# Performance work log

Measured on AMD Instinct MI355X. Metric: run time of the kernel, lower is better.

## Reference

```python
import jax, jax.numpy as jnp
import numpy as np
from jax.scipy.linalg import expm

D_LOGIC = 128
D_MEM = 16
SO_DIM = D_MEM * (D_MEM - 1) // 2  # 120


def _linear_init(key, fan_in, shape):
    bound = 1.0 / np.sqrt(fan_in)
    return jax.random.uniform(key, shape, jnp.float32, -bound, bound)


def setup_inputs() -> dict:
    key = jax.random.key(0)
    ks = jax.random.split(key, 14)
    B, S = 4, 128
    return {
        "x_logic": jax.random.normal(ks[0], (B, S, D_LOGIC), jnp.float32),
        "x_memory": jax.random.normal(ks[1], (B, S, D_MEM), jnp.float32),
        # W_Q / W_K
        "Wq": _linear_init(ks[2], D_LOGIC, (D_LOGIC, D_LOGIC)),
        "bq": _linear_init(ks[3], D_LOGIC, (D_LOGIC,)),
        "Wk": _linear_init(ks[4], D_LOGIC, (D_LOGIC, D_LOGIC)),
        "bk": _linear_init(ks[5], D_LOGIC, (D_LOGIC,)),
        # gamma_net: Linear(d_logic, 2*d_logic) -> Tanh -> Linear(2*d_logic, so_dim)
        "W1": _linear_init(ks[6], D_LOGIC, (2 * D_LOGIC, D_LOGIC)),
        "b1": _linear_init(ks[7], D_LOGIC, (2 * D_LOGIC,)),
        "W2": _linear_init(ks[8], 2 * D_LOGIC, (SO_DIM, 2 * D_LOGIC)),
        "b2": _linear_init(ks[9], 2 * D_LOGIC, (SO_DIM,)),
        # out_proj: Linear(d_memory, d_memory)
        "Wo": _linear_init(ks[10], D_MEM, (D_MEM, D_MEM)),
        "bo": _linear_init(ks[11], D_MEM, (D_MEM,)),
    }


def reference(x_logic, x_memory, Wq, bq, Wk, bk, W1, b1, W2, b2, Wo, bo):
    B, S, d_logic = x_logic.shape
    dm = x_memory.shape[-1]

    # attention over logic stream
    Q = x_logic @ Wq.T + bq
    K = x_logic @ Wk.T + bk
    attn = jax.nn.softmax(
        jnp.einsum("bjd,bid->bji", Q, K) / jnp.sqrt(jnp.float32(d_logic)), axis=-1
    )  # [B, S(j), S(i)]

    # per-pair Lie-algebra params: delta[b,j,i] = x_logic[b,j] - x_logic[b,i]
    delta = x_logic[:, :, None, :] - x_logic[:, None, :, :]  # [B,S,S,d_logic]
    h = jnp.tanh(delta @ W1.T + b1)
    lie = h @ W2.T + b2  # [B,S,S,so_dim]

    # scatter into skew-symmetric matrices [B,S,S,dm,dm]
    r, c = np.triu_indices(dm, k=1)
    skew = jnp.zeros((B, S, S, dm, dm), x_logic.dtype)
    skew = skew.at[..., r, c].set(lie)
    skew = skew.at[..., c, r].set(-lie)

    # Lie-group exponential -> orthogonal transport matrices
    T_all = expm(skew)  # [B,S,S,dm,dm]

    # transported[b,j,i,:] = T[b,j,i] @ x_memory[b,i]
    transported = jnp.einsum("bjide,bie->bjid", T_all, x_memory)

    # attention-weighted aggregation over i
    settled = jnp.einsum("bji,bjid->bjd", attn, transported)  # [B,S,dm]

    out = settled @ Wo.T + bo
    return out, T_all
```

## Files before the change

kernel.cpp:

```cpp
#include <hip/hip_runtime.h>
#include <hip/hip_fp16.h>

#define S_LEN 128
#define DLOG  128
#define DMEM  16
#define SO    120
#define HDIM  256

typedef _Float16 v8h __attribute__((ext_vector_type(8)));
typedef __fp16 v2hf __attribute__((ext_vector_type(2)));
typedef float v4f __attribute__((ext_vector_type(4)));

union PkU { v2hf h; unsigned u; };
union V8U { v8h v; int u[4]; };

__device__ __forceinline__ v8h splat8(float x) {
  _Float16 h = (_Float16)x;
  v8h v = {h, h, h, h, h, h, h, h};
  return v;
}

__global__ __launch_bounds__(512) void qku_kernel(
    const float* __restrict__ xl, const float* __restrict__ Wq,
    const float* __restrict__ bq, const float* __restrict__ Wk,
    const float* __restrict__ bk, const float* __restrict__ W1,
    float* __restrict__ Q, float* __restrict__ K, float* __restrict__ u) {
  int bj = blockIdx.x, t = threadIdx.x;
  int lane = t & 63, wu = t >> 6;
  int half = lane >> 5, l5 = lane & 31;
  float4 xv = *(const float4*)(xl + bj * 128 + 4 * l5);
  int seg = wu >> 1;
  const float* wb;
  if (seg == 0) wb = Wq;
  else if (seg == 1) wb = Wk - 128 * 128;
  else wb = W1 - 256 * 128;
  #pragma unroll 4
  for (int step = 0; step < 32; ++step) {
    int ro = wu * 64 + 2 * step + half;
    float4 wv = *(const float4*)(wb + ro * 128 + 4 * l5);
    float v = fmaf(wv.x, xv.x, fmaf(wv.y, xv.y, fmaf(wv.z, xv.z, wv.w * xv.w)));
    v += __shfl_xor(v, 1, 64);
    v += __shfl_xor(v, 2, 64);
    v += __shfl_xor(v, 4, 64);
    v += __shfl_xor(v, 8, 64);
    v += __shfl_xor(v, 16, 64);
    if (l5 == 0) {
      if (seg == 0) Q[bj * 128 + ro] = v + bq[ro];
      else if (seg == 1) K[bj * 128 + (ro - 128)] = v + bk[ro - 128];
      else u[bj * 256 + (ro - 256)] = v;
    }
  }
}

__global__ __launch_bounds__(128) void attn_kernel(
    const float* __restrict__ Q, const float* __restrict__ K,
    float* __restrict__ attn) {
  int bj = blockIdx.x, b = bj >> 7, t = threadIdx.x;
  int lane = t & 63, wu = t >> 6;
  int half = lane >> 5, l5 = lane & 31;
  __shared__ float sc[128];
  __shared__ float red[128];
  float4 qv = *(const float4*)(Q + bj * 128 + 4 * l5);
  #pragma unroll 4
  for (int step = 0; step < 32; ++step) {
    int ro = wu * 64 + 2 * step + half;
    float4 kv = *(const float4*)(K + (size_t)(b * 128 + ro) * 128 + 4 * l5);
    float v = fmaf(kv.x, qv.x, fmaf(kv.y, qv.y, fmaf(kv.z, qv.z, kv.w * qv.w)));
    v += __shfl_xor(v, 1, 64);
    v += __shfl_xor(v, 2, 64);
    v += __shfl_xor(v, 4, 64);
    v += __shfl_xor(v, 8, 64);
    v += __shfl_xor(v, 16, 64);
    if (l5 == 0) sc[ro] = v * 0.08838834764831845f;
  }
  __syncthreads();
  int i = t;
  float s = sc[i];
  red[i] = s;
  __syncthreads();
  for (int off = 64; off; off >>= 1) {
    if (i < off) red[i] = fmaxf(red[i], red[i + off]);
    __syncthreads();
  }
  float m = red[0];
  __syncthreads();
  float e = expf(s - m);
  red[i] = e;
  __syncthreads();
  for (int off = 64; off; off >>= 1) {
    if (i < off) red[i] += red[i + off];
    __syncthreads();
  }
  attn[(size_t)bj * 128 + i] = e / red[0];
}

__global__ __launch_bounds__(256) void h_from_u_kernel(
    const float* __restrict__ u, const float* __restrict__ b1,
    _Float16* __restrict__ hG, const float* __restrict__ W2g,
    _Float16* __restrict__ w2h) {
  if (blockIdx.x >= 2048) {
    int idx = ((blockIdx.x - 2048) * 256 + threadIdx.x) * 4;
    float4 v = *(const float4*)(W2g + idx);
    PkU u0, u1;
    u0.h = __builtin_amdgcn_cvt_pkrtz(v.x, v.y);
    u1.h = __builtin_amdgcn_cvt_pkrtz(v.z, v.w);
    uint2 pk = {u0.u, u1.u};
    *(uint2*)(w2h + idx) = pk;
    return;
  }
  int tid = blockIdx.x * 256 + threadIdx.x;
  #pragma unroll
  for (int g = 0; g < 4; ++g) {
    int unit = tid + g * 524288;
    int p = unit >> 5;
    int o0 = (unit & 31) * 8;
    int bj = p >> 7;
    int b = bj >> 7;
    int i = p & 127;
    const float* uj = u + bj * 256 + o0;
    const float* ui = u + (size_t)(b * 128 + i) * 256 + o0;
    const float* bb = b1 + o0;
    float4 j0 = *(const float4*)uj, j1 = *(const float4*)(uj + 4);
    float4 i0 = *(const float4*)ui, i1 = *(const float4*)(ui + 4);
    float4 c0 = *(const float4*)bb, c1 = *(const float4*)(bb + 4);
    float xv[8] = {j0.x - i0.x + c0.x, j0.y - i0.y + c0.y,
                   j0.z - i0.z + c0.z, j0.w - i0.w + c0.w,
                   j1.x - i1.x + c1.x, j1.y - i1.y + c1.y,
                   j1.z - i1.z + c1.z, j1.w - i1.w + c1.w};
    float rv[8];
    #pragma unroll
    for (int k = 0; k < 8; ++k) {
      float x = xv[k];
      float ax = fabsf(x);
      float e = __expf(-2.f * ax);
      float r = __fdividef(1.f - e, 1.f + e);
      rv[k] = copysignf(r, x);
    }
    V8U out;
    #pragma unroll
    for (int k = 0; k < 4; ++k) {
      PkU pu;
      pu.h = __builtin_amdgcn_cvt_pkrtz(rv[2 * k], rv[2 * k + 1]);
      out.u[k] = (int)pu.u;
    }
    *(v8h*)(hG + (size_t)p * 512 + o0) = out.v;
  }
}

__global__ __launch_bounds__(512) void lie_kernel(
    const _Float16* __restrict__ w2h, const float* __restrict__ b2g,
    float* __restrict__ Tg) {
  __shared__ _Float16 w2t[128 * 136];
  int t = threadIdx.x, lane = t & 63;
  int wu = __builtin_amdgcn_readfirstlane(t >> 6);
  int pbase = blockIdx.x * 128 + wu * 16;
  int nn = lane & 15, q = lane >> 4;
  const _Float16* hf = (const _Float16*)Tg;

  for (int idx = t; idx < 1088; idx += 512) w2t[16320 + idx] = (_Float16)0.f;

  v4f acc[8];
  #pragma unroll
  for (int tt = 0; tt < 8; ++tt) acc[tt] = (v4f){0.f, 0.f, 0.f, 0.f};

  const _Float16* hrow = hf + (size_t)(pbase + nn) * 512;
  for (int khalf = 0; khalf < 2; ++khalf) {
    __syncthreads();
    for (int idx = t; idx < 1920; idx += 512) {
      int row = idx >> 4, cu = (idx & 15) * 8;
      *(v8h*)(w2t + row * 136 + cu) =
          *(const v8h*)(w2h + row * 256 + khalf * 128 + cu);
    }
    __syncthreads();
    #pragma unroll
    for (int ks = 0; ks < 4; ++ks) {
      v8h ah = *(const v8h*)(hrow + khalf * 128 + ks * 32 + 8 * q);
      #pragma unroll
      for (int tt = 0; tt < 8; ++tt) {
        const v8h bf = *(const v8h*)(w2t + (16 * tt + nn) * 136 + ks * 32 + 8 * q);
        acc[tt] = __builtin_amdgcn_mfma_f32_16x16x32_f16(ah, bf, acc[tt], 0, 0, 0);
      }
    }
  }

  int rc0[8], rc1[8];
  float bbv[8];
  bool val[8];
  #pragma unroll
  for (int tt = 0; tt < 8; ++tt) {
    int n16 = 16 * tt + nn;
    val[tt] = (n16 < 120);
    float fr_ = floorf((31.0f - sqrtf(961.0f - 8.0f * (float)n16)) * 0.5f);
    int r = (int)fr_;
    int Sr = 15 * r - ((r * (r - 1)) >> 1);
    int c = n16 - Sr + r + 1;
    rc0[tt] = r * 16 + c;
    rc1[tt] = c * 16 + r;
    bbv[tt] = val[tt] ? b2g[n16] : 0.f;
  }

  _Float16* hw = (_Float16*)Tg;
  _Float16* aSt = w2t;
  for (int pass = 0; pass < 2; ++pass) {
    __syncthreads();
    #pragma unroll
    for (int reg = 0; reg < 4; ++reg) {
      int pidx = 4 * q + reg;
      if ((pidx >> 3) == pass) {
        _Float16* ab = aSt + (wu * 8 + (pidx & 7)) * 256;
        #pragma unroll
        for (int tt = 0; tt < 8; ++tt) {
          if (val[tt]) {
            _Float16 hv = (_Float16)(acc[tt][reg] + bbv[tt]);
            ab[rc0[tt]] = hv;
            ab[rc1[tt]] = -hv;
          }
        }
        ab[nn * 17] = (_Float16)0.f;
      }
    }
    __syncthreads();
    #pragma unroll
    for (int k = 0; k < 4; ++k) {
      int unit = t + k * 512;
      int lp = unit >> 5, off = (unit & 31) * 8;
      int g = blockIdx.x * 128 + (lp >> 3) * 16 + pass * 8 + (lp & 7);
      *(v8h*)(hw + (size_t)g * 512 + 256 + off) = *(const v8h*)(aSt + lp * 256 + off);
    }
  }
}

__device__ __forceinline__ void split8(const float* x, v8h& hi, v8h& lo) {
  union U { v8h v; v2hf p[4]; } H, L;
  #pragma unroll
  for (int i = 0; i < 4; ++i) {
    float a = x[2 * i], b = x[2 * i + 1];
    v2hf h = __builtin_amdgcn_cvt_pkrtz(a, b);
    float ra = (float)h[0], rb = (float)h[1];
    v2hf l = __builtin_amdgcn_cvt_pkrtz(a - ra, b - rb);
    H.p[i] = h;
    L.p[i] = l;
  }
  hi = H.v;
  lo = L.v;
}

__global__ __launch_bounds__(256) void expm_kernel(
    float* __restrict__ Tg, const float* __restrict__ attn,
    const float* __restrict__ xm, float* __restrict__ part) {
  __shared__ char lds[10240] __attribute__((aligned(16)));
  __shared__ float sred[4][16];
  int t = threadIdx.x, lane = t & 63;
  int wu = __builtin_amdgcn_readfirstlane(t >> 6);
  int pbase = blockIdx.x * 8 + wu * 2;
  int nn = lane & 15, q = lane >> 4, b8 = (q & 1) * 8;
  float* ErB = (float*)(lds + wu * 2560);
  const _Float16* hf = (const _Float16*)Tg;

  int idxA = ((2 * (q & 1)) * 16 + nn) * 4;
  int idxB = idxA + 64;

  float scv[2];
  int sv[2];
  V8U Apk[2], BfA[2];
  v4f Af[2];
  #pragma unroll
  for (int j = 0; j < 2; ++j) {
    size_t p = (size_t)(pbase + j);
    const _Float16* Ap = hf + p * 512 + 256;
    v8h rowh = *(const v8h*)(Ap + nn * 16 + b8);
    float s2 = 0.f;
    #pragma unroll
    for (int k = 0; k < 8; ++k) {
      float xf = (float)rowh[k];
      s2 = fmaf(xf, xf, s2);
    }
    #pragma unroll
    for (int off = 1; off < 64; off <<= 1) s2 += __shfl_xor(s2, off, 64);
    float bound = 0.5f * sqrtf(s2);
    int s = 0;
    while (bound > 1.0f && s < 12) { bound *= 0.5f; s++; }
    sv[j] = __builtin_amdgcn_readfirstlane(s);
    scv[j] = ldexpf(1.0f, -s);
    v8h sch = splat8(scv[j]);
    V8U ap;
    ap.v = rowh * sch;
    #pragma unroll
    for (int i = 0; i < 4; ++i) {
      Apk[j].u[i] = ap.u[i];
      BfA[j].u[i] = ap.u[i] ^ 0x80008000;
    }
    #pragma unroll
    for (int reg = 0; reg < 4; ++reg)
      Af[j][reg] = (float)Ap[(4 * q + reg) * 16 + nn] * scv[j];
  }

  V8U IC1, IC2;
  #pragma unroll
  for (int i = 0; i < 4; ++i) {
    float d0 = (b8 + 2 * i == nn) ? 1.f : 0.f;
    float d1 = (b8 + 2 * i + 1 == nn) ? 1.f : 0.f;
    PkU u1, u2;
    u1.h = __builtin_amdgcn_cvt_pkrtz(10.666667f * d0, 10.666667f * d1);
    u2.h = __builtin_amdgcn_cvt_pkrtz(2.1333333f * d0, 2.1333333f * d1);
    IC1.u[i] = (int)u1.u;
    IC2.u[i] = (int)u2.u;
  }

  v4f z4 = {0.f, 0.f, 0.f, 0.f};

  v4f cB[2];
  #pragma unroll
  for (int j = 0; j < 2; ++j)
    cB[j] = __builtin_amdgcn_mfma_f32_16x16x32_f16(Apk[j].v, BfA[j].v, z4, 0, 0, 0);

  V8U fB[2];
  #pragma unroll
  for (int j = 0; j < 2; ++j) {
    PkU u0, u1;
    u0.h = __builtin_amdgcn_cvt_pkrtz(cB[j][0], cB[j][1]);
    u1.h = __builtin_amdgcn_cvt_pkrtz(cB[j][2], cB[j][3]);
    fB[j].u[0] = __builtin_amdgcn_ds_bpermute(idxA, (int)u0.u);
    fB[j].u[1] = __builtin_amdgcn_ds_bpermute(idxA, (int)u1.u);
    fB[j].u[2] = __builtin_amdgcn_ds_bpermute(idxB, (int)u0.u);
    fB[j].u[3] = __builtin_amdgcn_ds_bpermute(idxB, (int)u1.u);
  }

  v4f cB2[2];
  #pragma unroll
  for (int j = 0; j < 2; ++j)
    cB2[j] = __builtin_amdgcn_mfma_f32_16x16x32_f16(fB[j].v, fB[j].v, z4, 0, 0, 0);

  V8U fB2[2];
  #pragma unroll
  for (int j = 0; j < 2; ++j) {
    PkU u0, u1;
    u0.h = __builtin_amdgcn_cvt_pkrtz(cB2[j][0], cB2[j][1]);
    u1.h = __builtin_amdgcn_cvt_pkrtz(cB2[j][2], cB2[j][3]);
    fB2[j].u[0] = __builtin_amdgcn_ds_bpermute(idxA, (int)u0.u);
    fB2[j].u[1] = __builtin_amdgcn_ds_bpermute(idxA, (int)u1.u);
    fB2[j].u[2] = __builtin_amdgcn_ds_bpermute(idxB, (int)u0.u);
    fB2[j].u[3] = __builtin_amdgcn_ds_bpermute(idxB, (int)u1.u);
  }

  v8h k1a = splat8(7.9365079e-4f);
  v8h k1b = splat8(0.17777778f);
  v8h k2a = splat8(8.8183422e-5f);
  v8h k2b = splat8(2.5396825e-2f);
  V8U M1[2], M2[2];
  #pragma unroll
  for (int j = 0; j < 2; ++j) {
    M1[j].v = fB2[j].v * k1a + (fB[j].v * k1b + IC1.v);
    M2[j].v = fB2[j].v * k2a + (fB[j].v * k2b + IC2.v);
  }

  v4f Cc[2], Qc[2];
  #pragma unroll
  for (int j = 0; j < 2; ++j) {
    v4f c3m = __builtin_amdgcn_mfma_f32_16x16x32_f16(M1[j].v, fB2[j].v, z4, 0, 0, 0);
    v4f c4m = __builtin_amdgcn_mfma_f32_16x16x32_f16(M2[j].v, fB2[j].v, z4, 0, 0, 0);
    #pragma unroll
    for (int reg = 0; reg < 4; ++reg) {
      float dg = (4 * q + reg == nn) ? 1.f : 0.f;
      Cc[j][reg] = fmaf(c3m[reg], 2.44140625e-4f,
                        fmaf(cB[j][reg], 0.25f, dg + Af[j][reg]));
      Qc[j][reg] = fmaf(c4m[reg], 2.44140625e-4f, cB[j][reg] * 0.083333333f);
    }
  }

  V8U fQ[2];
  #pragma unroll
  for (int j = 0; j < 2; ++j) {
    PkU u0, u1;
    u0.h = __builtin_amdgcn_cvt_pkrtz(Qc[j][0], Qc[j][1]);
    u1.h = __builtin_amdgcn_cvt_pkrtz(Qc[j][2], Qc[j][3]);
    fQ[j].u[0] = __builtin_amdgcn_ds_bpermute(idxA, (int)u0.u);
    fQ[j].u[1] = __builtin_amdgcn_ds_bpermute(idxA, (int)u1.u);
    fQ[j].u[2] = __builtin_amdgcn_ds_bpermute(idxB, (int)u0.u);
    fQ[j].u[3] = __builtin_amdgcn_ds_bpermute(idxB, (int)u1.u);
  }

  v4f E[2];
  #pragma unroll
  for (int j = 0; j < 2; ++j) {
    v4f c5 = __builtin_amdgcn_mfma_f32_16x16x32_f16(Apk[j].v, fQ[j].v, z4, 0, 0, 0);
    E[j] = Cc[j] + c5 * 0.5f;
  }

  int smax = max(sv[0], sv[1]);
  for (int it = 0; it < smax; ++it) {
    #pragma unroll
    for (int j = 0; j < 2; ++j) {
      if (it < sv[j]) {
        float* Erp = ErB + j * 320;
        PkU u0, u1;
        u0.h = __builtin_amdgcn_cvt_pkrtz(E[j][0], E[j][1]);
        u1.h = __builtin_amdgcn_cvt_pkrtz(E[j][2], E[j][3]);
        V8U bfe;
        bfe.u[0] = __builtin_amdgcn_ds_bpermute(idxA, (int)u0.u);
        bfe.u[1] = __builtin_amdgcn_ds_bpermute(idxA, (int)u1.u);
        bfe.u[2] = __builtin_amdgcn_ds_bpermute(idxB, (int)u0.u);
        bfe.u[3] = __builtin_amdgcn_ds_bpermute(idxB, (int)u1.u);
        #pragma unroll
        for (int reg = 0; reg < 4; ++reg)
          Erp[(4 * q + reg) * 20 + nn] = E[j][reg];
        asm volatile("s_waitcnt lgkmcnt(0)" ::: "memory");
        float4 a0 = *(const float4*)(Erp + nn * 20 + b8);
        float4 a1 = *(const float4*)(Erp + nn * 20 + b8 + 4);
        float xa[8] = {a0.x, a0.y, a0.z, a0.w, a1.x, a1.y, a1.z, a1.w};
        v8h ahi, alo;
        split8(xa, ahi, alo);
        v8h Ecat = (q < 2) ? ahi : alo;
        v4f z = {0.f, 0.f, 0.f, 0.f};
        E[j] = __builtin_amdgcn_mfma_f32_16x16x32_f16(Ecat, bfe.v, z, 0, 0, 0);
      }
    }
  }

  float pacc[4] = {0.f, 0.f, 0.f, 0.f};
  #pragma unroll
  for (int j = 0; j < 2; ++j) {
    int p = pbase + j;
    float* dst = Tg + (size_t)p * 256;
    #pragma unroll
    for (int reg = 0; reg < 4; ++reg)
      dst[(4 * q + reg) * 16 + nn] = E[j][reg];
    int b = p >> 14, i = p & 127;
    float xv = xm[((b << 7) + i) * 16 + nn];
    float aw = attn[(size_t)p] * xv;
    #pragma unroll
    for (int reg = 0; reg < 4; ++reg)
      pacc[reg] = fmaf(aw, E[j][reg], pacc[reg]);
  }
  #pragma unroll
  for (int reg = 0; reg < 4; ++reg) {
    #pragma unroll
    for (int off = 1; off < 16; off <<= 1)
      pacc[reg] += __shfl_xor(pacc[reg], off, 64);
  }
  if (nn == 0) {
    #pragma unroll
    for (int reg = 0; reg < 4; ++reg) sred[wu][4 * q + reg] = pacc[reg];
  }
  __syncthreads();
  if (t < 16)
    part[(size_t)blockIdx.x * 16 + t] =
        sred[0][t] + sred[1][t] + sred[2][t] + sred[3][t];
}

__global__ __launch_bounds__(64) void settle_fin_kernel(
    const float* __restrict__ part, const float* __restrict__ Wo,
    const float* __restrict__ bo, float* __restrict__ outp) {
  int bj = blockIdx.x, t = threadIdx.x;
  int r = t & 15, e0 = t >> 4;
  const float* pb = part + (size_t)bj * 256;
  float s = pb[e0 * 16 + r] + pb[(e0 + 4) * 16 + r] +
            pb[(e0 + 8) * 16 + r] + pb[(e0 + 12) * 16 + r];
  __shared__ float sf[64];
  sf[t] = s;
  __syncthreads();
  if (t < 16) sf[t] = sf[t] + sf[16 + t] + sf[32 + t] + sf[48 + t];
  __syncthreads();
  if (t < 16) {
    float o = bo[t];
    const float* wr = Wo + t * 16;
    #pragma unroll
    for (int c = 0; c < 16; ++c) o = fmaf(wr[c], sf[c], o);
    outp[bj * 16 + t] = o;
  }
}

extern "C" void kernel_launch(void* const* d_in, const int* in_sizes, int n_in,
                              void* d_out, int out_size, void* d_ws,
                              size_t ws_size, hipStream_t stream) {
  const float* xl = (const float*)d_in[0];
  const float* xm = (const float*)d_in[1];
  const float* Wq = (const float*)d_in[2];
  const float* bq = (const float*)d_in[3];
  const float* Wk = (const float*)d_in[4];
  const float* bk = (const float*)d_in[5];
  const float* W1 = (const float*)d_in[6];
  const float* b1 = (const float*)d_in[7];
  const float* W2 = (const float*)d_in[8];
  const float* b2 = (const float*)d_in[9];
  const float* Wo = (const float*)d_in[10];
  const float* bo = (const float*)d_in[11];
  float* outp = (float*)d_out;
  float* Tg = outp + 8192;
  float* wsf = (float*)d_ws;
  float* Q = wsf;
  float* K = wsf + 65536;
  float* attn = wsf + 131072;
  _Float16* w2h = (_Float16*)Q;
  float* u = wsf + 196608;
  float* part = wsf + 196608;

  hipLaunchKernelGGL(qku_kernel, dim3(512), dim3(512), 0, stream, xl, Wq, bq, Wk, bk, W1, Q, K, u);
  hipLaunchKernelGGL(attn_kernel, dim3(512), dim3(128), 0, stream, Q, K, attn);
  hipLaunchKernelGGL(h_from_u_kernel, dim3(2078), dim3(256), 0, stream, u, b1, (_Float16*)Tg, W2, w2h);
  hipLaunchKernelGGL(lie_kernel, dim3(512), dim3(512), 0, stream, w2h, b2, Tg);
  hipLaunchKernelGGL(expm_kernel, dim3(8192), dim3(256), 0, stream, Tg, attn, xm, part);
  hipLaunchKernelGGL(settle_fin_kernel, dim3(512), dim3(64), 0, stream, part, Wo, bo, outp);
}
```

Baseline: 201.6 us.

## Fuse lie projection into expm kernel and merge attention with tanh kernel

Merges the attention softmax and the tanh hidden-activation kernel into one launch, and fuses the W2 projection (lie_kernel) into the matrix-exponential kernel so skew matrices stay in LDS instead of round-tripping through global memory. Each expm block now handles 64 pairs in a loop, converting W2 to fp16 on the fly per block. The scaling bound now also uses an infinity-norm estimate (min with the Frobenius-based bound), which can reduce squaring steps. The cost is redundant W2 loading and conversion per block, plus larger LDS use that may lower occupancy.

```diff
diff --git a/kernel.cpp b/kernel.cpp
--- a/kernel.cpp
+++ b/kernel.cpp
@@ -52,63 +52,53 @@
   }
 }
 
-__global__ __launch_bounds__(128) void attn_kernel(
+__global__ __launch_bounds__(256) void attn_h_kernel(
     const float* __restrict__ Q, const float* __restrict__ K,
-    float* __restrict__ attn) {
-  int bj = blockIdx.x, b = bj >> 7, t = threadIdx.x;
-  int lane = t & 63, wu = t >> 6;
-  int half = lane >> 5, l5 = lane & 31;
-  __shared__ float sc[128];
-  __shared__ float red[128];
-  float4 qv = *(const float4*)(Q + bj * 128 + 4 * l5);
-  #pragma unroll 4
-  for (int step = 0; step < 32; ++step) {
-    int ro = wu * 64 + 2 * step + half;
-    float4 kv = *(const float4*)(K + (size_t)(b * 128 + ro) * 128 + 4 * l5);
-    float v = fmaf(kv.x, qv.x, fmaf(kv.y, qv.y, fmaf(kv.z, qv.z, kv.w * qv.w)));
-    v += __shfl_xor(v, 1, 64);
-    v += __shfl_xor(v, 2, 64);
-    v += __shfl_xor(v, 4, 64);
-    v += __shfl_xor(v, 8, 64);
-    v += __shfl_xor(v, 16, 64);
-    if (l5 == 0) sc[ro] = v * 0.08838834764831845f;
-  }
-  __syncthreads();
-  int i = t;
-  float s = sc[i];
-  red[i] = s;
-  __syncthreads();
-  for (int off = 64; off; off >>= 1) {
-    if (i < off) red[i] = fmaxf(red[i], red[i + off]);
-    __syncthreads();
-  }
-  float m = red[0];
-  __syncthreads();
-  float e = expf(s - m);
-  red[i] = e;
-  __syncthreads();
-  for (int off = 64; off; off >>= 1) {
-    if (i < off) red[i] += red[i + off];
-    __syncthreads();
-  }
-  attn[(size_t)bj * 128 + i] = e / red[0];
-}
-
-__global__ __launch_bounds__(256) void h_from_u_kernel(
-    const float* __restrict__ u, const float* __restrict__ b1,
-    _Float16* __restrict__ hG, const float* __restrict__ W2g,
-    _Float16* __restrict__ w2h) {
-  if (blockIdx.x >= 2048) {
-    int idx = ((blockIdx.x - 2048) * 256 + threadIdx.x) * 4;
-    float4 v = *(const float4*)(W2g + idx);
-    PkU u0, u1;
-    u0.h = __builtin_amdgcn_cvt_pkrtz(v.x, v.y);
-    u1.h = __builtin_amdgcn_cvt_pkrtz(v.z, v.w);
-    uint2 pk = {u0.u, u1.u};
-    *(uint2*)(w2h + idx) = pk;
+    float* __restrict__ attn, const float* __restrict__ u,
+    const float* __restrict__ b1, _Float16* __restrict__ hG) {
+  int t = threadIdx.x;
+  if (blockIdx.x < 256) {
+    int sub = t >> 7, t128 = t & 127;
+    int bj = blockIdx.x * 2 + sub, b = bj >> 7;
+    int lane = t & 63, wu = (t >> 6) & 1;
+    int half = lane >> 5, l5 = lane & 31;
+    __shared__ float sc[2][128];
+    __shared__ float red[2][128];
+    float4 qv = *(const float4*)(Q + bj * 128 + 4 * l5);
+    #pragma unroll 4
+    for (int step = 0; step < 32; ++step) {
+      int ro = wu * 64 + 2 * step + half;
+      float4 kv = *(const float4*)(K + (size_t)(b * 128 + ro) * 128 + 4 * l5);
+      float v = fmaf(kv.x, qv.x, fmaf(kv.y, qv.y, fmaf(kv.z, qv.z, kv.w * qv.w)));
+      v += __shfl_xor(v, 1, 64);
+      v += __shfl_xor(v, 2, 64);
+      v += __shfl_xor(v, 4, 64);
+      v += __shfl_xor(v, 8, 64);
+      v += __shfl_xor(v, 16, 64);
+      if (l5 == 0) sc[sub][ro] = v * 0.08838834764831845f;
+    }
+    __syncthreads();
+    int i = t128;
+    float s = sc[sub][i];
+    red[sub][i] = s;
+    __syncthreads();
+    for (int off = 64; off; off >>= 1) {
+      if (i < off) red[sub][i] = fmaxf(red[sub][i], red[sub][i + off]);
+      __syncthreads();
+    }
+    float m = red[sub][0];
+    __syncthreads();
+    float e = expf(s - m);
+    red[sub][i] = e;
+    __syncthreads();
+    for (int off = 64; off; off >>= 1) {
+      if (i < off) red[sub][i] += red[sub][i + off];
+      __syncthreads();
+    }
+    attn[(size_t)bj * 128 + i] = e / red[sub][0];
     return;
   }
-  int tid = blockIdx.x * 256 + threadIdx.x;
+  int tid = (blockIdx.x - 256) * 256 + t;
   #pragma unroll
   for (int g = 0; g < 4; ++g) {
     int unit = tid + g * 524288;
@@ -147,89 +137,6 @@
   }
 }
 
-__global__ __launch_bounds__(512) void lie_kernel(
-    const _Float16* __restrict__ w2h, const float* __restrict__ b2g,
-    float* __restrict__ Tg) {
-  __shared__ _Float16 w2t[128 * 136];
-  int t = threadIdx.x, lane = t & 63;
-  int wu = __builtin_amdgcn_readfirstlane(t >> 6);
-  int pbase = blockIdx.x * 128 + wu * 16;
-  int nn = lane & 15, q = lane >> 4;
-  const _Float16* hf = (const _Float16*)Tg;
-
-  for (int idx = t; idx < 1088; idx += 512) w2t[16320 + idx] = (_Float16)0.f;
-
-  v4f acc[8];
-  #pragma unroll
-  for (int tt = 0; tt < 8; ++tt) acc[tt] = (v4f){0.f, 0.f, 0.f, 0.f};
-
-  const _Float16* hrow = hf + (size_t)(pbase + nn) * 512;
-  for (int khalf = 0; khalf < 2; ++khalf) {
-    __syncthreads();
-    for (int idx = t; idx < 1920; idx += 512) {
-      int row = idx >> 4, cu = (idx & 15) * 8;
-      *(v8h*)(w2t + row * 136 + cu) =
-          *(const v8h*)(w2h + row * 256 + khalf * 128 + cu);
-    }
-    __syncthreads();
-    #pragma unroll
-    for (int ks = 0; ks < 4; ++ks) {
-      v8h ah = *(const v8h*)(hrow + khalf * 128 + ks * 32 + 8 * q);
-      #pragma unroll
-      for (int tt = 0; tt < 8; ++tt) {
-        const v8h bf = *(const v8h*)(w2t + (16 * tt + nn) * 136 + ks * 32 + 8 * q);
-        acc[tt] = __builtin_amdgcn_mfma_f32_16x16x32_f16(ah, bf, acc[tt], 0, 0, 0);
-      }
-    }
-  }
-
-  int rc0[8], rc1[8];
-  float bbv[8];
-  bool val[8];
-  #pragma unroll
-  for (int tt = 0; tt < 8; ++tt) {
-    int n16 = 16 * tt + nn;
-    val[tt] = (n16 < 120);
-    float fr_ = floorf((31.0f - sqrtf(961.0f - 8.0f * (float)n16)) * 0.5f);
-    int r = (int)fr_;
-    int Sr = 15 * r - ((r * (r - 1)) >> 1);
-    int c = n16 - Sr + r + 1;
-    rc0[tt] = r * 16 + c;
-    rc1[tt] = c * 16 + r;
-    bbv[tt] = val[tt] ? b2g[n16] : 0.f;
-  }
-
-  _Float16* hw = (_Float16*)Tg;
-  _Float16* aSt = w2t;
-  for (int pass = 0; pass < 2; ++pass) {
-    __syncthreads();
-    #pragma unroll
-    for (int reg = 0; reg < 4; ++reg) {
-      int pidx = 4 * q + reg;
-      if ((pidx >> 3) == pass) {
-        _Float16* ab = aSt + (wu * 8 + (pidx & 7)) * 256;
-        #pragma unroll
-        for (int tt = 0; tt < 8; ++tt) {
-          if (val[tt]) {
-            _Float16 hv = (_Float16)(acc[tt][reg] + bbv[tt]);
-            ab[rc0[tt]] = hv;
-            ab[rc1[tt]] = -hv;
-          }
-        }
-        ab[nn * 17] = (_Float16)0.f;
-      }
-    }
-    __syncthreads();
-    #pragma unroll
-    for (int k = 0; k < 4; ++k) {
-      int unit = t + k * 512;
-      int lp = unit >> 5, off = (unit & 31) * 8;
-      int g = blockIdx.x * 128 + (lp >> 3) * 16 + pass * 8 + (lp & 7);
-      *(v8h*)(hw + (size_t)g * 512 + 256 + off) = *(const v8h*)(aSt + lp * 256 + off);
-    }
-  }
-}
-
 __device__ __forceinline__ void split8(const float* x, v8h& hi, v8h& lo) {
   union U { v8h v; v2hf p[4]; } H, L;
   #pragma unroll
@@ -245,55 +152,76 @@
   lo = L.v;
 }
 
-__global__ __launch_bounds__(256) void expm_kernel(
+__global__ __launch_bounds__(256) void lie_expm_kernel(
+    const float* __restrict__ W2g, const float* __restrict__ b2g,
     float* __restrict__ Tg, const float* __restrict__ attn,
     const float* __restrict__ xm, float* __restrict__ part) {
-  __shared__ char lds[10240] __attribute__((aligned(16)));
+  __shared__ _Float16 w2t[128 * 136];
+  __shared__ float ErB_all[4 * 640];
   __shared__ float sred[4][16];
   int t = threadIdx.x, lane = t & 63;
   int wu = __builtin_amdgcn_readfirstlane(t >> 6);
-  int pbase = blockIdx.x * 8 + wu * 2;
   int nn = lane & 15, q = lane >> 4, b8 = (q & 1) * 8;
-  float* ErB = (float*)(lds + wu * 2560);
+  int gbase = blockIdx.x * 64;
   const _Float16* hf = (const _Float16*)Tg;
+
+  for (int idx = t; idx < 1088; idx += 256) w2t[16320 + idx] = (_Float16)0.f;
+
+  v4f acc[8];
+  #pragma unroll
+  for (int tt = 0; tt < 8; ++tt) acc[tt] = (v4f){0.f, 0.f, 0.f, 0.f};
+
+  const _Float16* hrow = hf + (size_t)(gbase + wu * 16 + nn) * 512;
+  for (int khalf = 0; khalf < 2; ++khalf) {
+    __syncthreads();
+    for (int idx = t; idx < 3840; idx += 256) {
+      int row = idx >> 5, c4 = (idx & 31) * 4;
+      float4 v = *(const float4*)(W2g + row * 256 + khalf * 128 + c4);
+      PkU a, b;
+      a.h = __builtin_amdgcn_cvt_pkrtz(v.x, v.y);
+      b.h = __builtin_amdgcn_cvt_pkrtz(v.z, v.w);
+      uint2 pk = {a.u, b.u};
+      *(uint2*)(w2t + row * 136 + c4) = pk;
+    }
+    __syncthreads();
+    #pragma unroll
+    for (int ks = 0; ks < 4; ++ks) {
+      v8h ah = *(const v8h*)(hrow + khalf * 128 + ks * 32 + 8 * q);
+      #pragma unroll
+      for (int tt = 0; tt < 8; ++tt) {
+        const v8h bf = *(const v8h*)(w2t + (16 * tt + nn) * 136 + ks * 32 + 8 * q);
+        acc[tt] = __builtin_amdgcn_mfma_f32_16x16x32_f16(ah, bf, acc[tt], 0, 0, 0);
+      }
+    }
+  }
+
+  __syncthreads();
+  _Float16* A = w2t;
+  #pragma unroll
+  for (int tt = 0; tt < 8; ++tt) {
+    int n16 = 16 * tt + nn;
+    if (n16 < 120) {
+      float bb = b2g[n16];
+      float fr_ = floorf((31.0f - sqrtf(961.0f - 8.0f * (float)n16)) * 0.5f);
+      int r = (int)fr_;
+      int Sr = 15 * r - ((r * (r - 1)) >> 1);
+      int c = n16 - Sr + r + 1;
+      #pragma unroll
+      for (int reg = 0; reg < 4; ++reg) {
+        int lp = wu * 16 + 4 * q + reg;
+        _Float16 hv = (_Float16)(acc[tt][reg] + bb);
+        A[lp * 256 + r * 16 + c] = hv;
+        A[lp * 256 + c * 16 + r] = -hv;
+      }
+    }
+  }
+  #pragma unroll
+  for (int reg = 0; reg < 4; ++reg)
+    A[(wu * 16 + 4 * q + reg) * 256 + nn * 17] = (_Float16)0.f;
 
   int idxA = ((2 * (q & 1)) * 16 + nn) * 4;
   int idxB = idxA + 64;
-
-  float scv[2];
-  int sv[2];
-  V8U Apk[2], BfA[2];
-  v4f Af[2];
-  #pragma unroll
-  for (int j = 0; j < 2; ++j) {
-    size_t p = (size_t)(pbase + j);
-    const _Float16* Ap = hf + p * 512 + 256;
-    v8h rowh = *(const v8h*)(Ap + nn * 16 + b8);
-    float s2 = 0.f;
-    #pragma unroll
-    for (int k = 0; k < 8; ++k) {
-      float xf = (float)rowh[k];
-      s2 = fmaf(xf, xf, s2);
-    }
-    #pragma unroll
-    for (int off = 1; off < 64; off <<= 1) s2 += __shfl_xor(s2, off, 64);
-    float bound = 0.5f * sqrtf(s2);
-    int s = 0;
-    while (bound > 1.0f && s < 12) { bound *= 0.5f; s++; }
-    sv[j] = __builtin_amdgcn_readfirstlane(s);
-    scv[j] = ldexpf(1.0f, -s);
-    v8h sch = splat8(scv[j]);
-    V8U ap;
-    ap.v = rowh * sch;
-    #pragma unroll
-    for (int i = 0; i < 4; ++i) {
-      Apk[j].u[i] = ap.u[i];
-      BfA[j].u[i] = ap.u[i] ^ 0x80008000;
-    }
-    #pragma unroll
-    for (int reg = 0; reg < 4; ++reg)
-      Af[j][reg] = (float)Ap[(4 * q + reg) * 16 + nn] * scv[j];
-  }
+  float* ErW = ErB_all + wu * 640;
 
   V8U IC1, IC2;
   #pragma unroll
@@ -306,132 +234,177 @@
     IC1.u[i] = (int)u1.u;
     IC2.u[i] = (int)u2.u;
   }
-
-  v4f z4 = {0.f, 0.f, 0.f, 0.f};
-
-  v4f cB[2];
-  #pragma unroll
-  for (int j = 0; j < 2; ++j)
-    cB[j] = __builtin_amdgcn_mfma_f32_16x16x32_f16(Apk[j].v, BfA[j].v, z4, 0, 0, 0);
-
-  V8U fB[2];
-  #pragma unroll
-  for (int j = 0; j < 2; ++j) {
-    PkU u0, u1;
-    u0.h = __builtin_amdgcn_cvt_pkrtz(cB[j][0], cB[j][1]);
-    u1.h = __builtin_amdgcn_cvt_pkrtz(cB[j][2], cB[j][3]);
-    fB[j].u[0] = __builtin_amdgcn_ds_bpermute(idxA, (int)u0.u);
-    fB[j].u[1] = __builtin_amdgcn_ds_bpermute(idxA, (int)u1.u);
-    fB[j].u[2] = __builtin_amdgcn_ds_bpermute(idxB, (int)u0.u);
-    fB[j].u[3] = __builtin_amdgcn_ds_bpermute(idxB, (int)u1.u);
-  }
-
-  v4f cB2[2];
-  #pragma unroll
-  for (int j = 0; j < 2; ++j)
-    cB2[j] = __builtin_amdgcn_mfma_f32_16x16x32_f16(fB[j].v, fB[j].v, z4, 0, 0, 0);
-
-  V8U fB2[2];
-  #pragma unroll
-  for (int j = 0; j < 2; ++j) {
-    PkU u0, u1;
-    u0.h = __builtin_amdgcn_cvt_pkrtz(cB2[j][0], cB2[j][1]);
-    u1.h = __builtin_amdgcn_cvt_pkrtz(cB2[j][2], cB2[j][3]);
-    fB2[j].u[0] = __builtin_amdgcn_ds_bpermute(idxA, (int)u0.u);
-    fB2[j].u[1] = __builtin_amdgcn_ds_bpermute(idxA, (int)u1.u);
-    fB2[j].u[2] = __builtin_amdgcn_ds_bpermute(idxB, (int)u0.u);
-    fB2[j].u[3] = __builtin_amdgcn_ds_bpermute(idxB, (int)u1.u);
-  }
-
   v8h k1a = splat8(7.9365079e-4f);
   v8h k1b = splat8(0.17777778f);
   v8h k2a = splat8(8.8183422e-5f);
   v8h k2b = splat8(2.5396825e-2f);
-  V8U M1[2], M2[2];
-  #pragma unroll
-  for (int j = 0; j < 2; ++j) {
-    M1[j].v = fB2[j].v * k1a + (fB[j].v * k1b + IC1.v);
-    M2[j].v = fB2[j].v * k2a + (fB[j].v * k2b + IC2.v);
-  }
-
-  v4f Cc[2], Qc[2];
-  #pragma unroll
-  for (int j = 0; j < 2; ++j) {
-    v4f c3m = __builtin_amdgcn_mfma_f32_16x16x32_f16(M1[j].v, fB2[j].v, z4, 0, 0, 0);
-    v4f c4m = __builtin_amdgcn_mfma_f32_16x16x32_f16(M2[j].v, fB2[j].v, z4, 0, 0, 0);
-    #pragma unroll
-    for (int reg = 0; reg < 4; ++reg) {
-      float dg = (4 * q + reg == nn) ? 1.f : 0.f;
-      Cc[j][reg] = fmaf(c3m[reg], 2.44140625e-4f,
-                        fmaf(cB[j][reg], 0.25f, dg + Af[j][reg]));
-      Qc[j][reg] = fmaf(c4m[reg], 2.44140625e-4f, cB[j][reg] * 0.083333333f);
-    }
-  }
-
-  V8U fQ[2];
-  #pragma unroll
-  for (int j = 0; j < 2; ++j) {
-    PkU u0, u1;
-    u0.h = __builtin_amdgcn_cvt_pkrtz(Qc[j][0], Qc[j][1]);
-    u1.h = __builtin_amdgcn_cvt_pkrtz(Qc[j][2], Qc[j][3]);
-    fQ[j].u[0] = __builtin_amdgcn_ds_bpermute(idxA, (int)u0.u);
-    fQ[j].u[1] = __builtin_amdgcn_ds_bpermute(idxA, (int)u1.u);
-    fQ[j].u[2] = __builtin_amdgcn_ds_bpermute(idxB, (int)u0.u);
-    fQ[j].u[3] = __builtin_amdgcn_ds_bpermute(idxB, (int)u1.u);
-  }
-
-  v4f E[2];
-  #pragma unroll
-  for (int j = 0; j < 2; ++j) {
-    v4f c5 = __builtin_amdgcn_mfma_f32_16x16x32_f16(Apk[j].v, fQ[j].v, z4, 0, 0, 0);
-    E[j] = Cc[j] + c5 * 0.5f;
-  }
-
-  int smax = max(sv[0], sv[1]);
-  for (int it = 0; it < smax; ++it) {
-    #pragma unroll
-    for (int j = 0; j < 2; ++j) {
-      if (it < sv[j]) {
-        float* Erp = ErB + j * 320;
-        PkU u0, u1;
-        u0.h = __builtin_amdgcn_cvt_pkrtz(E[j][0], E[j][1]);
-        u1.h = __builtin_amdgcn_cvt_pkrtz(E[j][2], E[j][3]);
-        V8U bfe;
-        bfe.u[0] = __builtin_amdgcn_ds_bpermute(idxA, (int)u0.u);
-        bfe.u[1] = __builtin_amdgcn_ds_bpermute(idxA, (int)u1.u);
-        bfe.u[2] = __builtin_amdgcn_ds_bpermute(idxB, (int)u0.u);
-        bfe.u[3] = __builtin_amdgcn_ds_bpermute(idxB, (int)u1.u);
-        #pragma unroll
-        for (int reg = 0; reg < 4; ++reg)
-          Erp[(4 * q + reg) * 20 + nn] = E[j][reg];
-        asm volatile("s_waitcnt lgkmcnt(0)" ::: "memory");
-        float4 a0 = *(const float4*)(Erp + nn * 20 + b8);
-        float4 a1 = *(const float4*)(Erp + nn * 20 + b8 + 4);
-        float xa[8] = {a0.x, a0.y, a0.z, a0.w, a1.x, a1.y, a1.z, a1.w};
-        v8h ahi, alo;
-        split8(xa, ahi, alo);
-        v8h Ecat = (q < 2) ? ahi : alo;
-        v4f z = {0.f, 0.f, 0.f, 0.f};
-        E[j] = __builtin_amdgcn_mfma_f32_16x16x32_f16(Ecat, bfe.v, z, 0, 0, 0);
-      }
-    }
-  }
+  v4f z4 = {0.f, 0.f, 0.f, 0.f};
 
   float pacc[4] = {0.f, 0.f, 0.f, 0.f};
-  #pragma unroll
-  for (int j = 0; j < 2; ++j) {
-    int p = pbase + j;
-    float* dst = Tg + (size_t)p * 256;
-    #pragma unroll
-    for (int reg = 0; reg < 4; ++reg)
-      dst[(4 * q + reg) * 16 + nn] = E[j][reg];
-    int b = p >> 14, i = p & 127;
-    float xv = xm[((b << 7) + i) * 16 + nn];
-    float aw = attn[(size_t)p] * xv;
-    #pragma unroll
-    for (int reg = 0; reg < 4; ++reg)
-      pacc[reg] = fmaf(aw, E[j][reg], pacc[reg]);
-  }
+
+  for (int pj = 0; pj < 8; ++pj) {
+    int lp0 = wu * 16 + pj * 2;
+
+    float scv[2];
+    int sv[2];
+    V8U Apk[2], BfA[2];
+    v4f Af[2];
+    #pragma unroll
+    for (int j = 0; j < 2; ++j) {
+      const _Float16* Ap = A + (lp0 + j) * 256;
+      v8h rowh = *(const v8h*)(Ap + nn * 16 + b8);
+      float s2 = 0.f, s1 = 0.f;
+      #pragma unroll
+      for (int k = 0; k < 8; ++k) {
+        float xf = (float)rowh[k];
+        s2 = fmaf(xf, xf, s2);
+        s1 += fabsf(xf);
+      }
+      s1 += __shfl_xor(s1, 16, 64);
+      s1 = fmaxf(s1, __shfl_xor(s1, 1, 64));
+      s1 = fmaxf(s1, __shfl_xor(s1, 2, 64));
+      s1 = fmaxf(s1, __shfl_xor(s1, 4, 64));
+      s1 = fmaxf(s1, __shfl_xor(s1, 8, 64));
+      #pragma unroll
+      for (int off = 1; off < 64; off <<= 1) s2 += __shfl_xor(s2, off, 64);
+      float bound = fminf(0.5f * sqrtf(s2), s1);
+      int s = 0;
+      while (bound > 1.0f && s < 12) { bound *= 0.5f; s++; }
+      sv[j] = __builtin_amdgcn_readfirstlane(s);
+      scv[j] = ldexpf(1.0f, -s);
+      v8h sch = splat8(scv[j]);
+      V8U ap;
+      ap.v = rowh * sch;
+      #pragma unroll
+      for (int i = 0; i < 4; ++i) {
+        Apk[j].u[i] = ap.u[i];
+        BfA[j].u[i] = ap.u[i] ^ 0x80008000;
+      }
+      #pragma unroll
+      for (int reg = 0; reg < 4; ++reg)
+        Af[j][reg] = (float)Ap[(4 * q + reg) * 16 + nn] * scv[j];
+    }
+
+    v4f cB[2];
+    #pragma unroll
+    for (int j = 0; j < 2; ++j)
+      cB[j] = __builtin_amdgcn_mfma_f32_16x16x32_f16(Apk[j].v, BfA[j].v, z4, 0, 0, 0);
+
+    V8U fB[2];
+    #pragma unroll
+    for (int j = 0; j < 2; ++j) {
+      PkU u0, u1;
+      u0.h = __builtin_amdgcn_cvt_pkrtz(cB[j][0], cB[j][1]);
+      u1.h = __builtin_amdgcn_cvt_pkrtz(cB[j][2], cB[j][3]);
+      fB[j].u[0] = __builtin_amdgcn_ds_bpermute(idxA, (int)u0.u);
+      fB[j].u[1] = __builtin_amdgcn_ds_bpermute(idxA, (int)u1.u);
+      fB[j].u[2] = __builtin_amdgcn_ds_bpermute(idxB, (int)u0.u);
+      fB[j].u[3] = __builtin_amdgcn_ds_bpermute(idxB, (int)u1.u);
+    }
+
+    v4f cB2[2];
+    #pragma unroll
+    for (int j = 0; j < 2; ++j)
+      cB2[j] = __builtin_amdgcn_mfma_f32_16x16x32_f16(fB[j].v, fB[j].v, z4, 0, 0, 0);
+
+    V8U fB2[2];
+    #pragma unroll
+    for (int j = 0; j < 2; ++j) {
+      PkU u0, u1;
+      u0.h = __builtin_amdgcn_cvt_pkrtz(cB2[j][0], cB2[j][1]);
+      u1.h = __builtin_amdgcn_cvt_pkrtz(cB2[j][2], cB2[j][3]);
+      fB2[j].u[0] = __builtin_amdgcn_ds_bpermute(idxA, (int)u0.u);
+      fB2[j].u[1] = __builtin_amdgcn_ds_bpermute(idxA, (int)u1.u);
+      fB2[j].u[2] = __builtin_amdgcn_ds_bpermute(idxB, (int)u0.u);
+      fB2[j].u[3] = __builtin_amdgcn_ds_bpermute(idxB, (int)u1.u);
+    }
+
+    V8U M1[2], M2[2];
+    #pragma unroll
+    for (int j = 0; j < 2; ++j) {
+      M1[j].v = fB2[j].v * k1a + (fB[j].v * k1b + IC1.v);
+      M2[j].v = fB2[j].v * k2a + (fB[j].v * k2b + IC2.v);
+    }
+
+    v4f Cc[2], Qc[2];
+    #pragma unroll
+    for (int j = 0; j < 2; ++j) {
+      v4f c3m = __builtin_amdgcn_mfma_f32_16x16x32_f16(M1[j].v, fB2[j].v, z4, 0, 0, 0);
+      v4f c4m = __builtin_amdgcn_mfma_f32_16x16x32_f16(M2[j].v, fB2[j].v, z4, 0, 0, 0);
+      #pragma unroll
+      for (int reg = 0; reg < 4; ++reg) {
+        float dg = (4 * q + reg == nn) ? 1.f : 0.f;
+        Cc[j][reg] = fmaf(c3m[reg], 2.44140625e-4f,
+                          fmaf(cB[j][reg], 0.25f, dg + Af[j][reg]));
+        Qc[j][reg] = fmaf(c4m[reg], 2.44140625e-4f, cB[j][reg] * 0.083333333f);
+      }
+    }
+
+    V8U fQ[2];
+    #pragma unroll
+    for (int j = 0; j < 2; ++j) {
+      PkU u0, u1;
+      u0.h = __builtin_amdgcn_cvt_pkrtz(Qc[j][0], Qc[j][1]);
+      u1.h = __builtin_amdgcn_cvt_pkrtz(Qc[j][2], Qc[j][3]);
+      fQ[j].u[0] = __builtin_amdgcn_ds_bpermute(idxA, (int)u0.u);
+      fQ[j].u[1] = __builtin_amdgcn_ds_bpermute(idxA, (int)u1.u);
+      fQ[j].u[2] = __builtin_amdgcn_ds_bpermute(idxB, (int)u0.u);
+      fQ[j].u[3] = __builtin_amdgcn_ds_bpermute(idxB, (int)u1.u);
+    }
+
+    v4f E[2];
+    #pragma unroll
+    for (int j = 0; j < 2; ++j) {
+      v4f c5 = __builtin_amdgcn_mfma_f32_16x16x32_f16(Apk[j].v, fQ[j].v, z4, 0, 0, 0);
+      E[j] = Cc[j] + c5 * 0.5f;
+    }
+
+    int smax = max(sv[0], sv[1]);
+    for (int it = 0; it < smax; ++it) {
+      #pragma unroll
+      for (int j = 0; j < 2; ++j) {
+        if (it < sv[j]) {
+          float* Erp = ErW + j * 320;
+          PkU u0, u1;
+          u0.h = __builtin_amdgcn_cvt_pkrtz(E[j][0], E[j][1]);
+          u1.h = __builtin_amdgcn_cvt_pkrtz(E[j][2], E[j][3]);
+          V8U bfe;
+          bfe.u[0] = __builtin_amdgcn_ds_bpermute(idxA, (int)u0.u);
+          bfe.u[1] = __builtin_amdgcn_ds_bpermute(idxA, (int)u1.u);
+          bfe.u[2] = __builtin_amdgcn_ds_bpermute(idxB, (int)u0.u);
+          bfe.u[3] = __builtin_amdgcn_ds_bpermute(idxB, (int)u1.u);
+          #pragma unroll
+          for (int reg = 0; reg < 4; ++reg)
+            Erp[(4 * q + reg) * 20 + nn] = E[j][reg];
+          asm volatile("s_waitcnt lgkmcnt(0)" ::: "memory");
+          float4 a0 = *(const float4*)(Erp + nn * 20 + b8);
+          float4 a1 = *(const float4*)(Erp + nn * 20 + b8 + 4);
+          float xa[8] = {a0.x, a0.y, a0.z, a0.w, a1.x, a1.y, a1.z, a1.w};
+          v8h ahi, alo;
+          split8(xa, ahi, alo);
+          v8h Ecat = (q < 2) ? ahi : alo;
+          v4f z = {0.f, 0.f, 0.f, 0.f};
+          E[j] = __builtin_amdgcn_mfma_f32_16x16x32_f16(Ecat, bfe.v, z, 0, 0, 0);
+        }
+      }
+    }
+
+    #pragma unroll
+    for (int j = 0; j < 2; ++j) {
+      int p = gbase + lp0 + j;
+      float* dst = Tg + (size_t)p * 256;
+      #pragma unroll
+      for (int reg = 0; reg < 4; ++reg)
+        dst[(4 * q + reg) * 16 + nn] = E[j][reg];
+      int b = p >> 14, i = p & 127;
+      float xv = xm[((b << 7) + i) * 16 + nn];
+      float aw = attn[(size_t)p] * xv;
+      #pragma unroll
+      for (int reg = 0; reg < 4; ++reg)
+        pacc[reg] = fmaf(aw, E[j][reg], pacc[reg]);
+    }
+  }
+
   #pragma unroll
   for (int reg = 0; reg < 4; ++reg) {
     #pragma unroll
@@ -452,14 +425,9 @@
     const float* __restrict__ part, const float* __restrict__ Wo,
     const float* __restrict__ bo, float* __restrict__ outp) {
   int bj = blockIdx.x, t = threadIdx.x;
-  int r = t & 15, e0 = t >> 4;
-  const float* pb = part + (size_t)bj * 256;
-  float s = pb[e0 * 16 + r] + pb[(e0 + 4) * 16 + r] +
-            pb[(e0 + 8) * 16 + r] + pb[(e0 + 12) * 16 + r];
-  __shared__ float sf[64];
-  sf[t] = s;
-  __syncthreads();
-  if (t < 16) sf[t] = sf[t] + sf[16 + t] + sf[32 + t] + sf[48 + t];
+  __shared__ float sf[16];
+  const float* pb = part + (size_t)bj * 32;
+  if (t < 16) sf[t] = pb[t] + pb[16 + t];
   __syncthreads();
   if (t < 16) {
     float o = bo[t];
@@ -491,14 +459,11 @@
   float* Q = wsf;
   float* K = wsf + 65536;
   float* attn = wsf + 131072;
-  _Float16* w2h = (_Float16*)Q;
   float* u = wsf + 196608;
   float* part = wsf + 196608;
 
   hipLaunchKernelGGL(qku_kernel, dim3(512), dim3(512), 0, stream, xl, Wq, bq, Wk, bk, W1, Q, K, u);
-  hipLaunchKernelGGL(attn_kernel, dim3(512), dim3(128), 0, stream, Q, K, attn);
-  hipLaunchKernelGGL(h_from_u_kernel, dim3(2078), dim3(256), 0, stream, u, b1, (_Float16*)Tg, W2, w2h);
-  hipLaunchKernelGGL(lie_kernel, dim3(512), dim3(512), 0, stream, w2h, b2, Tg);
-  hipLaunchKernelGGL(expm_kernel, dim3(8192), dim3(256), 0, stream, Tg, attn, xm, part);
+  hipLaunchKernelGGL(attn_h_kernel, dim3(2304), dim3(256), 0, stream, Q, K, attn, u, b1, (_Float16*)Tg);
+  hipLaunchKernelGGL(lie_expm_kernel, dim3(1024), dim3(256), 0, stream, W2, b2, Tg, attn, xm, part);
   hipLaunchKernelGGL(settle_fin_kernel, dim3(512), dim3(64), 0, stream, part, Wo, bo, outp);
 }
```

After: 202.8 us. No clear change (+0.6%).

## Merge attention and tanh kernels, convert W2 in lie kernel, tighten expm scaling bound

Applied to the files above, without the earlier changes.

Attention softmax and the tanh hidden-layer computation now run as two block ranges of a single launch, which removes one kernel launch. The separate fp32-to-fp16 conversion of W2 is dropped, and each lie_kernel block converts W2 as it loads it into shared memory, at the cost of reading it in fp32 in every block. The expm scaling bound now also uses a max-row-sum (1-norm style) estimate, so fewer squarings may be chosen. Taking the minimum of the two bounds is valid, but it lowers squaring counts, which could change accuracy slightly.

```diff
diff --git a/kernel.cpp b/kernel.cpp
--- a/kernel.cpp
+++ b/kernel.cpp
@@ -52,63 +52,53 @@
   }
 }
 
-__global__ __launch_bounds__(128) void attn_kernel(
+__global__ __launch_bounds__(256) void attn_h_kernel(
     const float* __restrict__ Q, const float* __restrict__ K,
-    float* __restrict__ attn) {
-  int bj = blockIdx.x, b = bj >> 7, t = threadIdx.x;
-  int lane = t & 63, wu = t >> 6;
-  int half = lane >> 5, l5 = lane & 31;
-  __shared__ float sc[128];
-  __shared__ float red[128];
-  float4 qv = *(const float4*)(Q + bj * 128 + 4 * l5);
-  #pragma unroll 4
-  for (int step = 0; step < 32; ++step) {
-    int ro = wu * 64 + 2 * step + half;
-    float4 kv = *(const float4*)(K + (size_t)(b * 128 + ro) * 128 + 4 * l5);
-    float v = fmaf(kv.x, qv.x, fmaf(kv.y, qv.y, fmaf(kv.z, qv.z, kv.w * qv.w)));
-    v += __shfl_xor(v, 1, 64);
-    v += __shfl_xor(v, 2, 64);
-    v += __shfl_xor(v, 4, 64);
-    v += __shfl_xor(v, 8, 64);
-    v += __shfl_xor(v, 16, 64);
-    if (l5 == 0) sc[ro] = v * 0.08838834764831845f;
-  }
-  __syncthreads();
-  int i = t;
-  float s = sc[i];
-  red[i] = s;
-  __syncthreads();
-  for (int off = 64; off; off >>= 1) {
-    if (i < off) red[i] = fmaxf(red[i], red[i + off]);
-    __syncthreads();
-  }
-  float m = red[0];
-  __syncthreads();
-  float e = expf(s - m);
-  red[i] = e;
-  __syncthreads();
-  for (int off = 64; off; off >>= 1) {
-    if (i < off) red[i] += red[i + off];
-    __syncthreads();
-  }
-  attn[(size_t)bj * 128 + i] = e / red[0];
-}
-
-__global__ __launch_bounds__(256) void h_from_u_kernel(
-    const float* __restrict__ u, const float* __restrict__ b1,
-    _Float16* __restrict__ hG, const float* __restrict__ W2g,
-    _Float16* __restrict__ w2h) {
-  if (blockIdx.x >= 2048) {
-    int idx = ((blockIdx.x - 2048) * 256 + threadIdx.x) * 4;
-    float4 v = *(const float4*)(W2g + idx);
-    PkU u0, u1;
-    u0.h = __builtin_amdgcn_cvt_pkrtz(v.x, v.y);
-    u1.h = __builtin_amdgcn_cvt_pkrtz(v.z, v.w);
-    uint2 pk = {u0.u, u1.u};
-    *(uint2*)(w2h + idx) = pk;
+    float* __restrict__ attn, const float* __restrict__ u,
+    const float* __restrict__ b1, _Float16* __restrict__ hG) {
+  int t = threadIdx.x;
+  if (blockIdx.x < 256) {
+    int sub = t >> 7, t128 = t & 127;
+    int bj = blockIdx.x * 2 + sub, b = bj >> 7;
+    int lane = t & 63, wu = (t >> 6) & 1;
+    int half = lane >> 5, l5 = lane & 31;
+    __shared__ float sc[2][128];
+    __shared__ float red[2][128];
+    float4 qv = *(const float4*)(Q + bj * 128 + 4 * l5);
+    #pragma unroll 4
+    for (int step = 0; step < 32; ++step) {
+      int ro = wu * 64 + 2 * step + half;
+      float4 kv = *(const float4*)(K + (size_t)(b * 128 + ro) * 128 + 4 * l5);
+      float v = fmaf(kv.x, qv.x, fmaf(kv.y, qv.y, fmaf(kv.z, qv.z, kv.w * qv.w)));
+      v += __shfl_xor(v, 1, 64);
+      v += __shfl_xor(v, 2, 64);
+      v += __shfl_xor(v, 4, 64);
+      v += __shfl_xor(v, 8, 64);
+      v += __shfl_xor(v, 16, 64);
+      if (l5 == 0) sc[sub][ro] = v * 0.08838834764831845f;
+    }
+    __syncthreads();
+    int i = t128;
+    float s = sc[sub][i];
+    red[sub][i] = s;
+    __syncthreads();
+    for (int off = 64; off; off >>= 1) {
+      if (i < off) red[sub][i] = fmaxf(red[sub][i], red[sub][i + off]);
+      __syncthreads();
+    }
+    float m = red[sub][0];
+    __syncthreads();
+    float e = expf(s - m);
+    red[sub][i] = e;
+    __syncthreads();
+    for (int off = 64; off; off >>= 1) {
+      if (i < off) red[sub][i] += red[sub][i + off];
+      __syncthreads();
+    }
+    attn[(size_t)bj * 128 + i] = e / red[sub][0];
     return;
   }
-  int tid = blockIdx.x * 256 + threadIdx.x;
+  int tid = (blockIdx.x - 256) * 256 + t;
   #pragma unroll
   for (int g = 0; g < 4; ++g) {
     int unit = tid + g * 524288;
@@ -148,7 +138,7 @@
 }
 
 __global__ __launch_bounds__(512) void lie_kernel(
-    const _Float16* __restrict__ w2h, const float* __restrict__ b2g,
+    const float* __restrict__ W2g, const float* __restrict__ b2g,
     float* __restrict__ Tg) {
   __shared__ _Float16 w2t[128 * 136];
   int t = threadIdx.x, lane = t & 63;
@@ -166,10 +156,14 @@
   const _Float16* hrow = hf + (size_t)(pbase + nn) * 512;
   for (int khalf = 0; khalf < 2; ++khalf) {
     __syncthreads();
-    for (int idx = t; idx < 1920; idx += 512) {
-      int row = idx >> 4, cu = (idx & 15) * 8;
-      *(v8h*)(w2t + row * 136 + cu) =
-          *(const v8h*)(w2h + row * 256 + khalf * 128 + cu);
+    for (int idx = t; idx < 3840; idx += 512) {
+      int row = idx >> 5, c4 = (idx & 31) * 4;
+      float4 v = *(const float4*)(W2g + row * 256 + khalf * 128 + c4);
+      PkU a, b;
+      a.h = __builtin_amdgcn_cvt_pkrtz(v.x, v.y);
+      b.h = __builtin_amdgcn_cvt_pkrtz(v.z, v.w);
+      uint2 pk = {a.u, b.u};
+      *(uint2*)(w2t + row * 136 + c4) = pk;
     }
     __syncthreads();
     #pragma unroll
@@ -269,15 +263,21 @@
     size_t p = (size_t)(pbase + j);
     const _Float16* Ap = hf + p * 512 + 256;
     v8h rowh = *(const v8h*)(Ap + nn * 16 + b8);
-    float s2 = 0.f;
+    float s2 = 0.f, s1 = 0.f;
     #pragma unroll
     for (int k = 0; k < 8; ++k) {
       float xf = (float)rowh[k];
       s2 = fmaf(xf, xf, s2);
-    }
+      s1 += fabsf(xf);
+    }
+    s1 += __shfl_xor(s1, 16, 64);
+    s1 = fmaxf(s1, __shfl_xor(s1, 1, 64));
+    s1 = fmaxf(s1, __shfl_xor(s1, 2, 64));
+    s1 = fmaxf(s1, __shfl_xor(s1, 4, 64));
+    s1 = fmaxf(s1, __shfl_xor(s1, 8, 64));
     #pragma unroll
     for (int off = 1; off < 64; off <<= 1) s2 += __shfl_xor(s2, off, 64);
-    float bound = 0.5f * sqrtf(s2);
+    float bound = fminf(0.5f * sqrtf(s2), s1);
     int s = 0;
     while (bound > 1.0f && s < 12) { bound *= 0.5f; s++; }
     sv[j] = __builtin_amdgcn_readfirstlane(s);
@@ -491,14 +491,12 @@
   float* Q = wsf;
   float* K = wsf + 65536;
   float* attn = wsf + 131072;
-  _Float16* w2h = (_Float16*)Q;
   float* u = wsf + 196608;
   float* part = wsf + 196608;
 
   hipLaunchKernelGGL(qku_kernel, dim3(512), dim3(512), 0, stream, xl, Wq, bq, Wk, bk, W1, Q, K, u);
-  hipLaunchKernelGGL(attn_kernel, dim3(512), dim3(128), 0, stream, Q, K, attn);
-  hipLaunchKernelGGL(h_from_u_kernel, dim3(2078), dim3(256), 0, stream, u, b1, (_Float16*)Tg, W2, w2h);
-  hipLaunchKernelGGL(lie_kernel, dim3(512), dim3(512), 0, stream, w2h, b2, Tg);
+  hipLaunchKernelGGL(attn_h_kernel, dim3(2304), dim3(256), 0, stream, Q, K, attn, u, b1, (_Float16*)Tg);
+  hipLaunchKernelGGL(lie_kernel, dim3(512), dim3(512), 0, stream, W2, b2, Tg);
   hipLaunchKernelGGL(expm_kernel, dim3(8192), dim3(256), 0, stream, Tg, attn, xm, part);
   hipLaunchKernelGGL(settle_fin_kernel, dim3(512), dim3(64), 0, stream, part, Wo, bo, outp);
 }
```

After: 196.6 us. 2.5% less time.
